# Optimization experiments

Measured on AMD Instinct MI355X. Metric: run time of the kernel, lower is better.

## Reference

```python
import jax, jax.numpy as jnp
import numpy as np

B, S, D = 8, 2048, 1024


def setup_inputs() -> dict:
    key = jax.random.key(0)
    ks = jax.random.split(key, 7)
    scale = 1.0 / np.sqrt(D)
    return {
        "tensor_sequence": jax.random.normal(ks[0], (B, S, D), dtype=jnp.float32),
        "Wq": jax.random.normal(ks[1], (D, D), dtype=jnp.float32) * scale,
        "bq": jax.random.normal(ks[2], (D,), dtype=jnp.float32) * scale,
        "Wk": jax.random.normal(ks[3], (D, D), dtype=jnp.float32) * scale,
        "bk": jax.random.normal(ks[4], (D,), dtype=jnp.float32) * scale,
        "Wv": jax.random.normal(ks[5], (D, D), dtype=jnp.float32) * scale,
        "bv": jax.random.normal(ks[6], (D,), dtype=jnp.float32) * scale,
    }


def reference(tensor_sequence, Wq, bq, Wk, bk, Wv, bv):
    # torch.nn.Linear: y = x @ W.T + b
    q = jnp.einsum("bsd,ed->bse", tensor_sequence, Wq) + bq
    k = jnp.einsum("bsd,ed->bse", tensor_sequence, Wk) + bk
    v = jnp.einsum("bsd,ed->bse", tensor_sequence, Wv) + bv
    scores = jnp.einsum("bqd,bkd->bqk", q, k)            # [B,S,S]
    weights = jax.nn.softmax(scores, axis=-1)
    attention = weights.sum(axis=-1)                      # [B,S] (== ones mathematically)
    out = jnp.einsum("bsf,bs->bf", v, attention)          # [B,D]
    return out
```

## Files before the change

kernel.cpp:

```cpp
#include <hip/hip_runtime.h>

#define BB 8
#define SS 2048
#define DD 1024
#define CH 128
#define RPC (SS / CH)
#define NI (BB * DD)
#define NI4 (NI / 4)


__global__ __launch_bounds__(256) void colsum_partial(
    const float* __restrict__ x, float* __restrict__ partial) {
    const int bid = blockIdx.x;
    const int b = bid >> 7;
    const int c = bid & (CH - 1);
    const int t = threadIdx.x;

    const float4* xp = (const float4*)(x + (size_t)b * SS * DD
                                         + (size_t)c * RPC * DD);
    float4 acc = make_float4(0.f, 0.f, 0.f, 0.f);
#pragma unroll
    for (int r = 0; r < RPC; ++r) {
        float4 v = xp[(size_t)r * (DD / 4) + t];
        acc.x += v.x; acc.y += v.y; acc.z += v.z; acc.w += v.w;
    }
    ((float4*)(partial + ((size_t)c * BB + b) * DD))[t] = acc;
}

__global__ __launch_bounds__(256) void colsum_reduce(
    const float* __restrict__ partial, float* __restrict__ xs) {
    const int ib = blockIdx.x;
    const int t = threadIdx.x;
    const int f4 = t & 7;
    const int cl = t >> 3;
    const int w  = t >> 6;
    const int lane = t & 63;

    const float4* p4 = (const float4*)partial;
    float4 a = make_float4(0.f, 0.f, 0.f, 0.f);
#pragma unroll
    for (int k = 0; k < CH / 32; ++k) {
        float4 v = p4[(size_t)(cl + 32 * k) * NI4 + ib * 8 + f4];
        a.x += v.x; a.y += v.y; a.z += v.z; a.w += v.w;
    }
#pragma unroll
    for (int off = 8; off <= 32; off <<= 1) {
        a.x += __shfl_xor(a.x, off);
        a.y += __shfl_xor(a.y, off);
        a.z += __shfl_xor(a.z, off);
        a.w += __shfl_xor(a.w, off);
    }
    __shared__ float4 lds[4][8];
    if ((lane >> 3) == 0) lds[w][f4] = a;
    __syncthreads();
    if (t < 8) {
        float4 s0 = lds[0][t], s1 = lds[1][t], s2 = lds[2][t], s3 = lds[3][t];
        float4 r;
        r.x = s0.x + s1.x + s2.x + s3.x;
        r.y = s0.y + s1.y + s2.y + s3.y;
        r.z = s0.z + s1.z + s2.z + s3.z;
        r.w = s0.w + s1.w + s2.w + s3.w;
        ((float4*)xs)[ib * 8 + t] = r;
    }
}

__global__ __launch_bounds__(256) void gemv_out(
    const float* __restrict__ Wv, const float* __restrict__ bv,
    const float* __restrict__ xs, float* __restrict__ out) {
    const int e = blockIdx.x;
    const int t = threadIdx.x;
    const int lane = t & 63;
    const int wid = t >> 6;

    const float4 w = ((const float4*)(Wv + (size_t)e * DD))[t];

    float acc[BB];
#pragma unroll
    for (int b = 0; b < BB; ++b) {
        float4 xv = ((const float4*)(xs + b * DD))[t];
        acc[b] = w.x * xv.x + w.y * xv.y + w.z * xv.z + w.w * xv.w;
    }

    __shared__ float lds[BB * 4];
#pragma unroll
    for (int b = 0; b < BB; ++b) {
        float v = acc[b];
#pragma unroll
        for (int off = 32; off > 0; off >>= 1) v += __shfl_down(v, off);
        if (lane == 0) lds[b * 4 + wid] = v;
    }
    __syncthreads();
    if (t < BB) {
        out[(size_t)t * DD + e] = lds[t * 4 + 0] + lds[t * 4 + 1]
                                + lds[t * 4 + 2] + lds[t * 4 + 3]
                                + (float)SS * bv[e];
    }
}

extern "C" void kernel_launch(void* const* d_in, const int* in_sizes, int n_in,
                              void* d_out, int out_size, void* d_ws, size_t ws_size,
                              hipStream_t stream) {
    const float* x  = (const float*)d_in[0];
    const float* Wv = (const float*)d_in[5];
    const float* bv = (const float*)d_in[6];
    float* out = (float*)d_out;

    float* partial = (float*)d_ws;
    float* xs      = partial + (size_t)CH * BB * DD;

    colsum_partial<<<BB * CH, 256, 0, stream>>>(x, partial);
    colsum_reduce<<<256, 256, 0, stream>>>(partial, xs);
    gemv_out<<<DD, 256, 0, stream>>>(Wv, bv, xs, out);
}
```

Measured before the change: 23.54 us.

## Fuse column-sum partial and reduce kernels into one direct column-tile reduction

Replaces the two-stage column sum (1024 row-chunk blocks writing partials, then a reduce kernel) with a single kernel. Each of 256 blocks owns a 32-column slice of one batch and walks all 2048 rows, then reduces across threads with shuffles and LDS. This drops the partial-buffer write/read and one kernel launch. In exchange it runs far fewer blocks, each streaming narrow 128-byte row segments at a 4 KB stride, which may reduce memory-level parallelism on the 64 MB input read.

```diff
diff --git a/kernel.cpp b/kernel.cpp
--- a/kernel.cpp
+++ b/kernel.cpp
@@ -3,44 +3,25 @@
 #define BB 8
 #define SS 2048
 #define DD 1024
-#define CH 128
-#define RPC (SS / CH)
-#define NI (BB * DD)
-#define NI4 (NI / 4)
 
 
-__global__ __launch_bounds__(256) void colsum_partial(
-    const float* __restrict__ x, float* __restrict__ partial) {
+__global__ __launch_bounds__(256) void colsum_direct(
+    const float* __restrict__ x, float* __restrict__ xs) {
     const int bid = blockIdx.x;
-    const int b = bid >> 7;
-    const int c = bid & (CH - 1);
-    const int t = threadIdx.x;
+    const int b  = bid >> 5;
+    const int dt = bid & 31;
+    const int t  = threadIdx.x;
+    const int f4 = t & 7;
+    const int rg = t >> 3;
+    const int lane = t & 63;
+    const int w  = t >> 6;
 
-    const float4* xp = (const float4*)(x + (size_t)b * SS * DD
-                                         + (size_t)c * RPC * DD);
-    float4 acc = make_float4(0.f, 0.f, 0.f, 0.f);
-#pragma unroll
-    for (int r = 0; r < RPC; ++r) {
-        float4 v = xp[(size_t)r * (DD / 4) + t];
-        acc.x += v.x; acc.y += v.y; acc.z += v.z; acc.w += v.w;
-    }
-    ((float4*)(partial + ((size_t)c * BB + b) * DD))[t] = acc;
-}
-
-__global__ __launch_bounds__(256) void colsum_reduce(
-    const float* __restrict__ partial, float* __restrict__ xs) {
-    const int ib = blockIdx.x;
-    const int t = threadIdx.x;
-    const int f4 = t & 7;
-    const int cl = t >> 3;
-    const int w  = t >> 6;
-    const int lane = t & 63;
-
-    const float4* p4 = (const float4*)partial;
+    const float* xb = x + (size_t)b * SS * DD + dt * 32;
     float4 a = make_float4(0.f, 0.f, 0.f, 0.f);
-#pragma unroll
-    for (int k = 0; k < CH / 32; ++k) {
-        float4 v = p4[(size_t)(cl + 32 * k) * NI4 + ib * 8 + f4];
+#pragma unroll 16
+    for (int it = 0; it < SS / 32; ++it) {
+        const int r = it * 32 + rg;
+        float4 v = ((const float4*)(xb + (size_t)r * DD))[f4];
         a.x += v.x; a.y += v.y; a.z += v.z; a.w += v.w;
     }
 #pragma unroll
@@ -51,16 +32,16 @@
         a.w += __shfl_xor(a.w, off);
     }
     __shared__ float4 lds[4][8];
-    if ((lane >> 3) == 0) lds[w][f4] = a;
+    if (lane < 8) lds[w][lane] = a;
     __syncthreads();
     if (t < 8) {
         float4 s0 = lds[0][t], s1 = lds[1][t], s2 = lds[2][t], s3 = lds[3][t];
-        float4 r;
-        r.x = s0.x + s1.x + s2.x + s3.x;
-        r.y = s0.y + s1.y + s2.y + s3.y;
-        r.z = s0.z + s1.z + s2.z + s3.z;
-        r.w = s0.w + s1.w + s2.w + s3.w;
-        ((float4*)xs)[ib * 8 + t] = r;
+        float4 r4;
+        r4.x = s0.x + s1.x + s2.x + s3.x;
+        r4.y = s0.y + s1.y + s2.y + s3.y;
+        r4.z = s0.z + s1.z + s2.z + s3.z;
+        r4.w = s0.w + s1.w + s2.w + s3.w;
+        ((float4*)xs)[bid * 8 + t] = r4;
     }
 }
 
@@ -105,10 +86,8 @@
     const float* bv = (const float*)d_in[6];
     float* out = (float*)d_out;
 
-    float* partial = (float*)d_ws;
-    float* xs      = partial + (size_t)CH * BB * DD;
+    float* xs = (float*)d_ws;
 
-    colsum_partial<<<BB * CH, 256, 0, stream>>>(x, partial);
-    colsum_reduce<<<256, 256, 0, stream>>>(partial, xs);
+    colsum_direct<<<BB * 32, 256, 0, stream>>>(x, xs);
     gemv_out<<<DD, 256, 0, stream>>>(Wv, bv, xs, out);
 }
```

Result: faster. 21.26 us (median of 2 runs) (-9.7%).
